# Optimization experiments

Hardware: AMD Instinct MI355X
Metric: run time of the kernel (lower is better)

Reference implementation:

```python
import jax, jax.numpy as jnp
import numpy as np

KP_THRESHOLD = 20.0
KP_BETA = 0.5
TARGET_ENTROPY = 6.0
LOG2 = 0.6931471805599453

B, C, H, W = 8, 18, 256, 256
N_HYP, K = 1024, 9


def setup_inputs() -> dict:
    key = jax.random.key(0)
    ks = jax.random.split(key, 16)
    inp = {}
    for i, sfx in enumerate(['_L', '_R']):
        o = 8 * i
        inp['vertex_pred' + sfx] = jax.random.normal(ks[o + 0], (B, C, H, W), jnp.float32)
        inp['vertex_gt' + sfx] = jax.random.normal(ks[o + 1], (B, C, H, W), jnp.float32)
        inp['mask' + sfx] = jax.random.randint(ks[o + 2], (B, H, W), 0, 2, jnp.int32)
        inp['seg' + sfx] = jax.random.normal(ks[o + 3], (B, 2, H, W), jnp.float32)
        inp['keypoints' + sfx] = jax.random.normal(ks[o + 4], (B, N_HYP, K, 2), jnp.float32) * 10.0
        inp['scores' + sfx] = jax.random.normal(ks[o + 5], (B, N_HYP, K), jnp.float32)
        inp['kpt_2d' + sfx] = jax.random.normal(ks[o + 6], (B, K, 2), jnp.float32) * 10.0
        inp['offset' + sfx] = jax.random.normal(ks[o + 7], (B, 2), jnp.float32)
    inp['softmax_a'] = jnp.asarray(0.5, jnp.float32)
    inp['epoch'] = 100
    return inp


def _smooth_l1_sum(x, y):
    d = jnp.abs(x - y)
    return jnp.sum(jnp.where(d < 1.0, 0.5 * d * d, d - 0.5))


def _side_losses(vertex_pred, vertex_gt, mask, seg, keypoints, scores, kpt_2d, a):
    w = mask[:, None].astype(jnp.float32)                      # [B,1,H,W]
    vote = _smooth_l1_sum(vertex_pred * w, vertex_gt * w)
    ws = jnp.sum(w)
    vote = jnp.where(ws > 0, vote / jnp.maximum(ws, 1.0) / vertex_gt.shape[1], vote)
    # CrossEntropyLoss (mean over B*H*W pixels)
    logp = jax.nn.log_softmax(seg, axis=1)                     # [B,2,H,W]
    nll = -jnp.take_along_axis(logp, mask[:, None], axis=1)[:, 0]
    seg_loss = jnp.mean(nll)
    # DSAC expected keypoint loss: softmax over hypothesis axis
    probs = jax.nn.softmax(a * scores, axis=1)                 # [B,N,K]
    dist = jnp.linalg.norm(keypoints - kpt_2d[:, None], axis=-1)
    kp_loss = jnp.mean(jnp.sum(probs * dist, axis=1))
    # entropy loss on detached scores (entropy in bits)
    s = jax.lax.stop_gradient(a * scores)
    p = jax.nn.softmax(s, axis=1)
    lp = jax.nn.log_softmax(s, axis=1) / LOG2
    entropy = jnp.mean(-jnp.sum(p * lp, axis=1), axis=1)       # [B]
    ent_loss = jnp.sum(jnp.abs(entropy - TARGET_ENTROPY)) / scores.shape[0]
    return vote, seg_loss, kp_loss, ent_loss


def _epipolar(kp_L, off_L, sc_L, kp_R, off_R, sc_R, a):
    # keypoints detached; add per-image crop offsets -> global coords
    kp_L = jax.lax.stop_gradient(kp_L) + off_L[:, None, None, :]
    kp_R = jax.lax.stop_gradient(kp_R) + off_R[:, None, None, :]
    kL, kR = jax.random.split(jax.random.key(1234))
    idx_L = jax.random.categorical(kL, jax.lax.stop_gradient(a * sc_L), axis=1)  # [B,K]
    idx_R = jax.random.categorical(kR, jax.lax.stop_gradient(a * sc_R), axis=1)
    yL = jnp.take_along_axis(kp_L[..., 1], idx_L[:, None, :], axis=1)[:, 0]      # [B,K]
    yR = jnp.take_along_axis(kp_R[..., 1], idx_R[:, None, :], axis=1)[:, 0]
    d = jnp.abs(yL - yR)  # sqrt((yL-yR)^2)
    d = jnp.where(jnp.isfinite(d), d, 0.0)
    return jnp.mean(d)    # mean over K then over B == global mean


def reference(vertex_pred_L, vertex_gt_L, mask_L, seg_L, keypoints_L, scores_L, kpt_2d_L, offset_L,
              vertex_pred_R, vertex_gt_R, mask_R, seg_R, keypoints_R, scores_R, kpt_2d_R, offset_R,
              softmax_a, epoch):
    vL, sL, kL, eL = _side_losses(vertex_pred_L, vertex_gt_L, mask_L, seg_L, keypoints_L, scores_L, kpt_2d_L, softmax_a)
    vR, sR, kR, eR = _side_losses(vertex_pred_R, vertex_gt_R, mask_R, seg_R, keypoints_R, scores_R, kpt_2d_R, softmax_a)
    vote_loss = (vL + vR) * 0.5
    seg_loss = (sL + sR) * 0.5
    kp_loss = (kL + kR) * 0.5
    entropy_loss = (eL + eR) * 0.5
    kp_w = jax.nn.sigmoid(KP_BETA * (KP_THRESHOLD - jax.lax.stop_gradient(kp_loss)))
    vote_w = 1.0 - kp_w
    if epoch > 49:
        epi = _epipolar(keypoints_L, offset_L, scores_L, keypoints_R, offset_R, scores_R, softmax_a)
        vertex_loss = kp_w * (kp_loss + epi) + vote_w * vote_loss
    else:
        vertex_loss = kp_w * kp_loss + vote_w * vote_loss
    loss = vertex_loss + entropy_loss + seg_loss
    return loss
```

## Files before the change

### kernel.cpp

```cpp
#include <hip/hip_runtime.h>
#include <stdint.h>
#include <math.h>

#define HWPIX 65536
#define NCH   18
#define NHYP  1024
#define NK    9
#define NBK   72
#define NPIXBLK 512
#define NGRP  6
#define CPG   3
#define INV_LOG2 1.4426950408889634f
#define TINYF 1.1754943508222875e-38f

#define OFS_VOTE 64
#define OFS_CNT  (OFS_VOTE + 2 * NGRP * NPIXBLK)
#define OFS_SEG  (OFS_CNT  + 2 * NPIXBLK)
#define OFS_KP   (OFS_SEG  + 2 * NPIXBLK)
#define OFS_ENT  (OFS_KP   + 2 * NBK)
#define OFS_Y    (OFS_ENT  + 2 * NBK)

__host__ __device__ inline void tf2x32(uint32_t k0, uint32_t k1,
                                       uint32_t x0, uint32_t x1,
                                       uint32_t& o0, uint32_t& o1) {
  uint32_t ks2 = k0 ^ k1 ^ 0x1BD11BDAu;
  x0 += k0; x1 += k1;
#define TFR(r) { x0 += x1; x1 = (x1 << (r)) | (x1 >> (32 - (r))); x1 ^= x0; }
  TFR(13) TFR(15) TFR(26) TFR(6)   x0 += k1;  x1 += ks2 + 1u;
  TFR(17) TFR(29) TFR(16) TFR(24)  x0 += ks2; x1 += k0 + 2u;
  TFR(13) TFR(15) TFR(26) TFR(6)   x0 += k0;  x1 += k1 + 3u;
  TFR(17) TFR(29) TFR(16) TFR(24)  x0 += k1;  x1 += ks2 + 4u;
  TFR(13) TFR(15) TFR(26) TFR(6)   x0 += ks2; x1 += k0 + 5u;
#undef TFR
  o0 = x0; o1 = x1;
}

__device__ inline float blk_sum(float v, float* sm) {
  int t = threadIdx.x;
  sm[t] = v; __syncthreads();
  for (int off = 128; off > 0; off >>= 1) {
    if (t < off) sm[t] += sm[t + off];
    __syncthreads();
  }
  float r = sm[0]; __syncthreads();
  return r;
}

__device__ inline float nll2(float s0, float s1, int lbl) {
  const float mx = fmaxf(s0, s1);
  const float mn = fminf(s0, s1);
  const float l = mx + logf(1.0f + expf(mn - mx));
  return l - (lbl ? s1 : s0);
}

__global__ __launch_bounds__(256) void pixel_kernel(
    const float* __restrict__ vpL, const float* __restrict__ vgL,
    const int*   __restrict__ mkL, const float* __restrict__ sgL,
    const float* __restrict__ vpR, const float* __restrict__ vgR,
    const int*   __restrict__ mkR, const float* __restrict__ sgR,
    float* __restrict__ ws) {
  const int side = blockIdx.z;
  const int grp  = blockIdx.y;
  const float* vp = side ? vpR : vpL;
  const float* vg = side ? vgR : vgL;
  const int*   mk = side ? mkR : mkL;
  const float* sg = side ? sgR : sgL;

  const int g  = blockIdx.x * 256 + threadIdx.x;
  const int p0 = g * 4;
  const int b  = p0 >> 16;
  const int hw = p0 & (HWPIX - 1);

  const int4 m4 = *(const int4*)(mk + p0);
  const float w0 = (float)m4.x, w1 = (float)m4.y, w2 = (float)m4.z, w3 = (float)m4.w;

  float4 p[CPG], q[CPG];
  const size_t vbase = (size_t)b * (NCH * HWPIX) + (size_t)(grp * CPG) * HWPIX + hw;
#pragma unroll
  for (int c = 0; c < CPG; ++c) p[c] = *(const float4*)(vp + vbase + (size_t)c * HWPIX);
#pragma unroll
  for (int c = 0; c < CPG; ++c) q[c] = *(const float4*)(vg + vbase + (size_t)c * HWPIX);

  float vote = 0.f;
#pragma unroll
  for (int c = 0; c < CPG; ++c) {
    float dd;
    dd = fabsf(p[c].x - q[c].x) * w0; vote += (dd < 1.f) ? 0.5f * dd * dd : dd - 0.5f;
    dd = fabsf(p[c].y - q[c].y) * w1; vote += (dd < 1.f) ? 0.5f * dd * dd : dd - 0.5f;
    dd = fabsf(p[c].z - q[c].z) * w2; vote += (dd < 1.f) ? 0.5f * dd * dd : dd - 0.5f;
    dd = fabsf(p[c].w - q[c].w) * w3; vote += (dd < 1.f) ? 0.5f * dd * dd : dd - 0.5f;
  }

  __shared__ float sm[256];
  const float v = blk_sum(vote, sm);
  if (threadIdx.x == 0)
    ws[OFS_VOTE + (side * NGRP + grp) * NPIXBLK + blockIdx.x] = v;

  if (grp == 0) {
    const float cnt = w0 + w1 + w2 + w3;
    const size_t sbase = (size_t)b * (2 * HWPIX) + hw;
    const float4 s0 = *(const float4*)(sg + sbase);
    const float4 s1 = *(const float4*)(sg + sbase + HWPIX);
    float seg = 0.f;
    seg += nll2(s0.x, s1.x, m4.x);
    seg += nll2(s0.y, s1.y, m4.y);
    seg += nll2(s0.z, s1.z, m4.z);
    seg += nll2(s0.w, s1.w, m4.w);
    const float c2 = blk_sum(cnt, sm);
    const float sg2 = blk_sum(seg, sm);
    if (threadIdx.x == 0) {
      ws[OFS_CNT + side * NPIXBLK + blockIdx.x] = c2;
      ws[OFS_SEG + side * NPIXBLK + blockIdx.x] = sg2;
    }
  }
}

__global__ __launch_bounds__(256) void hyp_kernel(
    const float* __restrict__ scL, const float* __restrict__ kpL,
    const float* __restrict__ k2L, const float* __restrict__ ofL,
    const float* __restrict__ scR, const float* __restrict__ kpR,
    const float* __restrict__ k2R, const float* __restrict__ ofR,
    const float* __restrict__ aPtr,
    uint32_t kLa, uint32_t kLb, uint32_t kRa, uint32_t kRb,
    float* __restrict__ ws) {
  const int side = blockIdx.y;
  const float* sc = side ? scR : scL;
  const float* kp = side ? kpR : kpL;
  const float* k2 = side ? k2R : k2L;
  const float* of = side ? ofR : ofL;
  const uint32_t K0 = side ? kRa : kLa;
  const uint32_t K1 = side ? kRb : kLb;
  const int bk = blockIdx.x;
  const int b = bk / NK, k = bk % NK;
  const int t = threadIdx.x;
  const float a = aPtr[0];
  const float kx = k2[(b * NK + k) * 2 + 0];
  const float ky = k2[(b * NK + k) * 2 + 1];
  const float2* kp2 = (const float2*)kp;

  float s[4], d[4], gv[4];
#pragma unroll
  for (int j = 0; j < 4; ++j) {
    const int n = t + j * 256;
    const size_t idx = ((size_t)b * NHYP + n) * NK + k;
    s[j] = a * sc[idx];
    const float2 xy = kp2[idx];
    const float dx = xy.x - kx, dy = xy.y - ky;
    d[j] = sqrtf(dx * dx + dy * dy);
    uint32_t o0, o1;
    tf2x32(K0, K1, 0u, (uint32_t)idx, o0, o1);
    const uint32_t bits = o0 ^ o1;
    float u = __uint_as_float((bits >> 9) | 0x3F800000u) - 1.0f;
    u = fmaxf(TINYF, u * (1.0f - TINYF) + TINYF);
    gv[j] = -logf(-logf(u)) + s[j];
  }

  __shared__ float sm[256];
  __shared__ int   si[256];

  float mx = fmaxf(fmaxf(s[0], s[1]), fmaxf(s[2], s[3]));
  sm[t] = mx; __syncthreads();
  for (int off = 128; off > 0; off >>= 1) {
    if (t < off) sm[t] = fmaxf(sm[t], sm[t + off]);
    __syncthreads();
  }
  mx = sm[0]; __syncthreads();

  float Z = 0.f, Sd = 0.f, Ss = 0.f;
#pragma unroll
  for (int j = 0; j < 4; ++j) {
    const float e = expf(s[j] - mx);
    Z  += e;
    Sd += e * d[j];
    Ss += e * (s[j] - mx);
  }
  Z  = blk_sum(Z, sm);
  Sd = blk_sum(Sd, sm);
  Ss = blk_sum(Ss, sm);

  float bv = gv[0]; int bi = t;
#pragma unroll
  for (int j = 1; j < 4; ++j) {
    const int n = t + j * 256;
    if (gv[j] > bv) { bv = gv[j]; bi = n; }
  }
  sm[t] = bv; si[t] = bi; __syncthreads();
  for (int off = 128; off > 0; off >>= 1) {
    if (t < off) {
      const float v2 = sm[t + off]; const int i2 = si[t + off];
      if (v2 > sm[t] || (v2 == sm[t] && i2 < si[t])) { sm[t] = v2; si[t] = i2; }
    }
    __syncthreads();
  }

  if (t == 0) {
    ws[OFS_KP  + side * NBK + bk] = Sd / Z;
    ws[OFS_ENT + side * NBK + bk] = (logf(Z) - Ss / Z) * INV_LOG2;
    const int n = si[0];
    ws[OFS_Y + side * NBK + bk] =
        kp2[((size_t)b * NHYP + n) * NK + k].y + of[b * 2 + 1];
  }
}

__global__ __launch_bounds__(256) void final_kernel(
    const int* __restrict__ epochPtr, const float* __restrict__ ws,
    float* __restrict__ out) {
  __shared__ float sm[256];
  const int t = threadIdx.x;
  float voteS[2], cntS[2], segS[2], kpS[2], entS[2];
  for (int side = 0; side < 2; ++side) {
    float a;
    a = 0.f;
    for (int j = t; j < NGRP * NPIXBLK; j += 256)
      a += ws[OFS_VOTE + side * NGRP * NPIXBLK + j];
    voteS[side] = blk_sum(a, sm);
    a = 0.f; for (int j = t; j < NPIXBLK; j += 256) a += ws[OFS_CNT + side * NPIXBLK + j];
    cntS[side] = blk_sum(a, sm);
    a = 0.f; for (int j = t; j < NPIXBLK; j += 256) a += ws[OFS_SEG + side * NPIXBLK + j];
    segS[side] = blk_sum(a, sm);
    a = (t < NBK) ? ws[OFS_KP + side * NBK + t] : 0.f;
    kpS[side] = blk_sum(a, sm);
    a = 0.f;
    if (t < 8) {
      float es = 0.f;
      for (int k = 0; k < NK; ++k) es += ws[OFS_ENT + side * NBK + t * NK + k];
      a = fabsf(es / (float)NK - 6.0f);
    }
    entS[side] = blk_sum(a, sm);
  }
  float e = 0.f;
  if (t < NBK) {
    const float dy = fabsf(ws[OFS_Y + t] - ws[OFS_Y + NBK + t]);
    e = isfinite(dy) ? dy : 0.f;
  }
  const float epiSum = blk_sum(e, sm);

  if (t == 0) {
    const float voteL = (cntS[0] > 0.f) ? voteS[0] / fmaxf(cntS[0], 1.f) / (float)NCH : voteS[0];
    const float voteR = (cntS[1] > 0.f) ? voteS[1] / fmaxf(cntS[1], 1.f) / (float)NCH : voteS[1];
    const float segL = segS[0] / 524288.f;
    const float segR = segS[1] / 524288.f;
    const float kpLm = kpS[0] / (float)NBK, kpRm = kpS[1] / (float)NBK;
    const float entL = entS[0] / 8.f, entR = entS[1] / 8.f;

    const float vote_loss = 0.5f * (voteL + voteR);
    const float seg_loss  = 0.5f * (segL + segR);
    const float kp_loss   = 0.5f * (kpLm + kpRm);
    const float ent_loss  = 0.5f * (entL + entR);
    const float kp_w  = 1.f / (1.f + expf(-0.5f * (20.f - kp_loss)));
    const float vote_w = 1.f - kp_w;
    float vertex;
    if (epochPtr[0] > 49) {
      const float epi = epiSum / (float)NBK;
      vertex = kp_w * (kp_loss + epi) + vote_w * vote_loss;
    } else {
      vertex = kp_w * kp_loss + vote_w * vote_loss;
    }
    out[0] = vertex + ent_loss + seg_loss;
  }
}

extern "C" void kernel_launch(void* const* d_in, const int* in_sizes, int n_in,
                              void* d_out, int out_size, void* d_ws, size_t ws_size,
                              hipStream_t stream) {
  (void)in_sizes; (void)n_in; (void)out_size; (void)ws_size;
  const float* vpL = (const float*)d_in[0];
  const float* vgL = (const float*)d_in[1];
  const int*   mkL = (const int*)  d_in[2];
  const float* sgL = (const float*)d_in[3];
  const float* kpL = (const float*)d_in[4];
  const float* scL = (const float*)d_in[5];
  const float* k2L = (const float*)d_in[6];
  const float* ofL = (const float*)d_in[7];
  const float* vpR = (const float*)d_in[8];
  const float* vgR = (const float*)d_in[9];
  const int*   mkR = (const int*)  d_in[10];
  const float* sgR = (const float*)d_in[11];
  const float* kpR = (const float*)d_in[12];
  const float* scR = (const float*)d_in[13];
  const float* k2R = (const float*)d_in[14];
  const float* ofR = (const float*)d_in[15];
  const float* aP  = (const float*)d_in[16];
  const int*   epP = (const int*)  d_in[17];
  float* ws  = (float*)d_ws;
  float* out = (float*)d_out;

  uint32_t kLa, kLb, kRa, kRb;
  tf2x32(0u, 1234u, 0u, 0u, kLa, kLb);
  tf2x32(0u, 1234u, 0u, 1u, kRa, kRb);

  pixel_kernel<<<dim3(NPIXBLK, NGRP, 2), 256, 0, stream>>>(
      vpL, vgL, mkL, sgL, vpR, vgR, mkR, sgR, ws);
  hyp_kernel<<<dim3(NBK, 2), 256, 0, stream>>>(
      scL, kpL, k2L, ofL, scR, kpR, k2R, ofR, aP, kLa, kLb, kRa, kRb, ws);
  final_kernel<<<1, 256, 0, stream>>>(epP, ws, out);
}
```

Before: 55.75 us.

## Split seg loss into its own kernel and flatten vote loop with batched loads

The pixel kernel is restructured so that each thread processes 9 float4 quads across a flattened side/plane index space in 3 batches of 3. All loads in a batch are issued before any compute, with a sched_barrier between them to keep them grouped. The segmentation cross-entropy and mask count move into a separate seg_kernel, which removes the divergent grp==0 branch and its extra block reductions from the vote blocks. This aims to raise memory-level parallelism and cut reduction overhead. In exchange it adds a kernel launch and reloads the mask per channel plane.

```diff
diff --git a/kernel.cpp b/kernel.cpp
--- a/kernel.cpp
+++ b/kernel.cpp
@@ -7,16 +7,16 @@
 #define NHYP  1024
 #define NK    9
 #define NBK   72
-#define NPIXBLK 512
-#define NGRP  6
-#define CPG   3
 #define INV_LOG2 1.4426950408889634f
 #define TINYF 1.1754943508222875e-38f
 
+#define NVBLK 2048
+#define VITER 9
+#define NSBLK 512
 #define OFS_VOTE 64
-#define OFS_CNT  (OFS_VOTE + 2 * NGRP * NPIXBLK)
-#define OFS_SEG  (OFS_CNT  + 2 * NPIXBLK)
-#define OFS_KP   (OFS_SEG  + 2 * NPIXBLK)
+#define OFS_CNT  (OFS_VOTE + 2 * NVBLK)
+#define OFS_SEG  (OFS_CNT  + 2 * NSBLK)
+#define OFS_KP   (OFS_SEG  + 2 * NSBLK)
 #define OFS_ENT  (OFS_KP   + 2 * NBK)
 #define OFS_Y    (OFS_ENT  + 2 * NBK)
 
@@ -46,6 +46,11 @@
   return r;
 }
 
+__device__ inline float sl1(float x, float y, float w) {
+  const float dd = fabsf(x - y) * w;
+  return (dd < 1.f) ? 0.5f * dd * dd : dd - 0.5f;
+}
+
 __device__ inline float nll2(float s0, float s1, int lbl) {
   const float mx = fmaxf(s0, s1);
   const float mn = fminf(s0, s1);
@@ -55,63 +60,97 @@
 
 __global__ __launch_bounds__(256) void pixel_kernel(
     const float* __restrict__ vpL, const float* __restrict__ vgL,
-    const int*   __restrict__ mkL, const float* __restrict__ sgL,
+    const int*   __restrict__ mkL,
     const float* __restrict__ vpR, const float* __restrict__ vgR,
-    const int*   __restrict__ mkR, const float* __restrict__ sgR,
+    const int*   __restrict__ mkR,
     float* __restrict__ ws) {
-  const int side = blockIdx.z;
-  const int grp  = blockIdx.y;
-  const float* vp = side ? vpR : vpL;
-  const float* vg = side ? vgR : vgL;
-  const int*   mk = side ? mkR : mkL;
-  const float* sg = side ? sgR : sgL;
-
-  const int g  = blockIdx.x * 256 + threadIdx.x;
-  const int p0 = g * 4;
-  const int b  = p0 >> 16;
-  const int hw = p0 & (HWPIX - 1);
-
-  const int4 m4 = *(const int4*)(mk + p0);
-  const float w0 = (float)m4.x, w1 = (float)m4.y, w2 = (float)m4.z, w3 = (float)m4.w;
-
-  float4 p[CPG], q[CPG];
-  const size_t vbase = (size_t)b * (NCH * HWPIX) + (size_t)(grp * CPG) * HWPIX + hw;
-#pragma unroll
-  for (int c = 0; c < CPG; ++c) p[c] = *(const float4*)(vp + vbase + (size_t)c * HWPIX);
-#pragma unroll
-  for (int c = 0; c < CPG; ++c) q[c] = *(const float4*)(vg + vbase + (size_t)c * HWPIX);
-
-  float vote = 0.f;
-#pragma unroll
-  for (int c = 0; c < CPG; ++c) {
-    float dd;
-    dd = fabsf(p[c].x - q[c].x) * w0; vote += (dd < 1.f) ? 0.5f * dd * dd : dd - 0.5f;
-    dd = fabsf(p[c].y - q[c].y) * w1; vote += (dd < 1.f) ? 0.5f * dd * dd : dd - 0.5f;
-    dd = fabsf(p[c].z - q[c].z) * w2; vote += (dd < 1.f) ? 0.5f * dd * dd : dd - 0.5f;
-    dd = fabsf(p[c].w - q[c].w) * w3; vote += (dd < 1.f) ? 0.5f * dd * dd : dd - 0.5f;
+  const int tid = blockIdx.x * 256 + threadIdx.x;
+  float vL = 0.f, vR = 0.f;
+
+#pragma unroll
+  for (int batch = 0; batch < 3; ++batch) {
+    int4 m4[3]; float4 p4[3], q4[3]; int sd[3];
+#pragma unroll
+    for (int j = 0; j < 3; ++j) {
+      const int Fq    = tid + (batch * 3 + j) * (NVBLK * 256);
+      const int plane = Fq >> 14;
+      const int hwq   = Fq & 16383;
+      const int side  = plane >= 144;
+      const int lp    = plane - side * 144;
+      const int b     = lp / 18;
+      const float* vp = side ? vpR : vpL;
+      const float* vg = side ? vgR : vgL;
+      const int*   mk = side ? mkR : mkL;
+      const size_t voff = ((size_t)lp << 16) + ((size_t)hwq << 2);
+      m4[j] = *(const int4*)(mk + ((size_t)b << 16) + ((size_t)hwq << 2));
+      p4[j] = *(const float4*)(vp + voff);
+      q4[j] = *(const float4*)(vg + voff);
+      sd[j] = side;
+    }
+    __builtin_amdgcn_sched_barrier(0);
+#pragma unroll
+    for (int j = 0; j < 3; ++j) {
+      float v = 0.f;
+      v += sl1(p4[j].x, q4[j].x, (float)m4[j].x);
+      v += sl1(p4[j].y, q4[j].y, (float)m4[j].y);
+      v += sl1(p4[j].z, q4[j].z, (float)m4[j].z);
+      v += sl1(p4[j].w, q4[j].w, (float)m4[j].w);
+      vL += sd[j] ? 0.f : v;
+      vR += sd[j] ? v : 0.f;
+    }
   }
 
   __shared__ float sm[256];
-  const float v = blk_sum(vote, sm);
-  if (threadIdx.x == 0)
-    ws[OFS_VOTE + (side * NGRP + grp) * NPIXBLK + blockIdx.x] = v;
-
-  if (grp == 0) {
-    const float cnt = w0 + w1 + w2 + w3;
-    const size_t sbase = (size_t)b * (2 * HWPIX) + hw;
-    const float4 s0 = *(const float4*)(sg + sbase);
-    const float4 s1 = *(const float4*)(sg + sbase + HWPIX);
-    float seg = 0.f;
-    seg += nll2(s0.x, s1.x, m4.x);
-    seg += nll2(s0.y, s1.y, m4.y);
-    seg += nll2(s0.z, s1.z, m4.z);
-    seg += nll2(s0.w, s1.w, m4.w);
-    const float c2 = blk_sum(cnt, sm);
-    const float sg2 = blk_sum(seg, sm);
-    if (threadIdx.x == 0) {
-      ws[OFS_CNT + side * NPIXBLK + blockIdx.x] = c2;
-      ws[OFS_SEG + side * NPIXBLK + blockIdx.x] = sg2;
-    }
+  const float rL = blk_sum(vL, sm);
+  const float rR = blk_sum(vR, sm);
+  if (threadIdx.x == 0) {
+    ws[OFS_VOTE + blockIdx.x]         = rL;
+    ws[OFS_VOTE + NVBLK + blockIdx.x] = rR;
+  }
+}
+
+__global__ __launch_bounds__(256) void seg_kernel(
+    const int* __restrict__ mkL, const float* __restrict__ sgL,
+    const int* __restrict__ mkR, const float* __restrict__ sgR,
+    float* __restrict__ ws) {
+  const int tid = blockIdx.x * 256 + threadIdx.x;
+  float cnt[2], seg[2];
+
+  int4 m4[2]; float4 s0[2], s1[2];
+#pragma unroll
+  for (int it = 0; it < 2; ++it) {
+    const int*   mk = it ? mkR : mkL;
+    const float* sg = it ? sgR : sgL;
+    const int b   = tid >> 14;
+    const int hwq = tid & 16383;
+    const size_t moff = ((size_t)b << 16) + ((size_t)hwq << 2);
+    const size_t soff = ((size_t)b << 17) + ((size_t)hwq << 2);
+    m4[it] = *(const int4*)(mk + moff);
+    s0[it] = *(const float4*)(sg + soff);
+    s1[it] = *(const float4*)(sg + soff + HWPIX);
+  }
+  __builtin_amdgcn_sched_barrier(0);
+#pragma unroll
+  for (int it = 0; it < 2; ++it) {
+    cnt[it] = (float)(m4[it].x + m4[it].y + m4[it].z + m4[it].w);
+    float s = 0.f;
+    s += nll2(s0[it].x, s1[it].x, m4[it].x);
+    s += nll2(s0[it].y, s1[it].y, m4[it].y);
+    s += nll2(s0[it].z, s1[it].z, m4[it].z);
+    s += nll2(s0[it].w, s1[it].w, m4[it].w);
+    seg[it] = s;
+  }
+
+  __shared__ float sm[256];
+  const float c0 = blk_sum(cnt[0], sm);
+  const float c1 = blk_sum(cnt[1], sm);
+  const float g0 = blk_sum(seg[0], sm);
+  const float g1 = blk_sum(seg[1], sm);
+  if (threadIdx.x == 0) {
+    ws[OFS_CNT + blockIdx.x]         = c0;
+    ws[OFS_CNT + NSBLK + blockIdx.x] = c1;
+    ws[OFS_SEG + blockIdx.x]         = g0;
+    ws[OFS_SEG + NSBLK + blockIdx.x] = g1;
   }
 }
 
@@ -210,13 +249,11 @@
   float voteS[2], cntS[2], segS[2], kpS[2], entS[2];
   for (int side = 0; side < 2; ++side) {
     float a;
-    a = 0.f;
-    for (int j = t; j < NGRP * NPIXBLK; j += 256)
-      a += ws[OFS_VOTE + side * NGRP * NPIXBLK + j];
+    a = 0.f; for (int j = t; j < NVBLK; j += 256) a += ws[OFS_VOTE + side * NVBLK + j];
     voteS[side] = blk_sum(a, sm);
-    a = 0.f; for (int j = t; j < NPIXBLK; j += 256) a += ws[OFS_CNT + side * NPIXBLK + j];
+    a = 0.f; for (int j = t; j < NSBLK; j += 256) a += ws[OFS_CNT + side * NSBLK + j];
     cntS[side] = blk_sum(a, sm);
-    a = 0.f; for (int j = t; j < NPIXBLK; j += 256) a += ws[OFS_SEG + side * NPIXBLK + j];
+    a = 0.f; for (int j = t; j < NSBLK; j += 256) a += ws[OFS_SEG + side * NSBLK + j];
     segS[side] = blk_sum(a, sm);
     a = (t < NBK) ? ws[OFS_KP + side * NBK + t] : 0.f;
     kpS[side] = blk_sum(a, sm);
@@ -289,8 +326,8 @@
   tf2x32(0u, 1234u, 0u, 0u, kLa, kLb);
   tf2x32(0u, 1234u, 0u, 1u, kRa, kRb);
 
-  pixel_kernel<<<dim3(NPIXBLK, NGRP, 2), 256, 0, stream>>>(
-      vpL, vgL, mkL, sgL, vpR, vgR, mkR, sgR, ws);
+  pixel_kernel<<<NVBLK, 256, 0, stream>>>(vpL, vgL, mkL, vpR, vgR, mkR, ws);
+  seg_kernel<<<NSBLK, 256, 0, stream>>>(mkL, sgL, mkR, sgR, ws);
   hyp_kernel<<<dim3(NBK, 2), 256, 0, stream>>>(
       scL, kpL, k2L, ofL, scR, kpR, k2R, ofR, aP, kLa, kLb, kRa, kRb, ws);
   final_kernel<<<1, 256, 0, stream>>>(epP, ws, out);
```

Result: slower. 59.66 us (+7.0%).
